# Kernel tuning notes

Hardware: AMD Instinct MI355X
Metric: run time of the kernel (lower is better)

The kernel has to match this reference:

```python
import jax, jax.numpy as jnp
import numpy as np

C = 256
EPS = 1e-5


def setup_inputs() -> dict:
    key = jax.random.key(0)
    ks = jax.random.split(key, 10)
    B, H, W = 4, 64, 64
    x1 = jax.random.normal(ks[0], (B, C, H, W), dtype=jnp.float32)
    x2 = jax.random.normal(ks[1], (B, C, H, W), dtype=jnp.float32)
    s = 1.0 / np.sqrt(C)
    qw = jax.random.normal(ks[2], (C, C), dtype=jnp.float32) * s
    qb = jax.random.normal(ks[3], (C,), dtype=jnp.float32) * 0.01
    kw = jax.random.normal(ks[4], (C, C), dtype=jnp.float32) * s
    kb = jax.random.normal(ks[5], (C,), dtype=jnp.float32) * 0.01
    vw = jax.random.normal(ks[6], (C, C), dtype=jnp.float32) * s
    vb = jax.random.normal(ks[7], (C,), dtype=jnp.float32) * 0.01
    ln_w = jnp.ones((C,), dtype=jnp.float32)
    ln_b = jnp.zeros((C,), dtype=jnp.float32)
    return {"x1": x1, "x2": x2, "qw": qw, "qb": qb, "kw": kw, "kb": kb,
            "vw": vw, "vb": vb, "ln_w": ln_w, "ln_b": ln_b}


def _conv1x1(x, w, b):
    # 1x1 conv == per-pixel matmul over channels. x: [B,C,H,W], w: [O,C]
    return jnp.einsum('oc,bchw->bohw', w, x) + b[None, :, None, None]


def reference(x1, x2, qw, qb, kw, kb, vw, vb, ln_w, ln_b):
    q = _conv1x1(x1, qw, qb)   # [B,C,H,W]
    k = _conv1x1(x2, kw, kb)   # [B,C,H,W]
    v = _conv1x1(x2, vw, vb)   # [B,C,H,W]
    # scores: [B,H,W,I,J]; softmax over LAST axis (j) only, as in the torch code
    scores = jnp.einsum('bchw,bcij->bhwij', q, k)
    attn = jax.nn.softmax(scores, axis=-1)
    fusion = jnp.einsum('bhwij,bcij->bchw', attn, v)  # [B,C,H,W]
    # LayerNorm2d: normalize over channel dim per spatial location
    mean = jnp.mean(fusion, axis=1, keepdims=True)
    var = jnp.var(fusion, axis=1, keepdims=True)
    normed = (fusion - mean) * jax.lax.rsqrt(var + EPS)
    return normed * ln_w[None, :, None, None] + ln_b[None, :, None, None]
```

## Files before the change

### kernel.cpp

```cpp
#include <hip/hip_runtime.h>


#define CDIM 256
#define NPOS 4096
#define BATCH 4
#define EPSV 1e-5f

typedef _Float16 f16;
typedef __attribute__((ext_vector_type(4))) _Float16 f16x4;
typedef __attribute__((ext_vector_type(8))) _Float16 f16x8;
typedef __attribute__((ext_vector_type(4))) float f32x4;
typedef __attribute__((ext_vector_type(16))) float f32x16;

#define WST       264
#define QK_STRIDE 264
#define V_STRIDE  72
#define DQ_STRIDE 72
#define F_STRIDE  68

#define LBAR() asm volatile("s_waitcnt lgkmcnt(0)\n\ts_barrier" ::: "memory")


static __device__ __forceinline__ f16x8 cvt8(const float* __restrict__ p) {
    float4 w0 = *(const float4*)p;
    float4 w1 = *(const float4*)(p + 4);
    f16x8 r;
    r[0] = (f16)w0.x; r[1] = (f16)w0.y; r[2] = (f16)w0.z; r[3] = (f16)w0.w;
    r[4] = (f16)w1.x; r[5] = (f16)w1.y; r[6] = (f16)w1.z; r[7] = (f16)w1.w;
    return r;
}

__global__ __launch_bounds__(256, 4) void prep_kernel(
    const float* __restrict__ x1, const float* __restrict__ x2,
    const float* __restrict__ qw, const float* __restrict__ kw,
    const float* __restrict__ vw,
    f16* __restrict__ X1T, f16* __restrict__ X2T, f16* __restrict__ W16)
{
    const int id = blockIdx.x;
    const int t  = threadIdx.x;
    if (id < 2048) {
        __shared__ f16 T[64 * 72];
        const float* xs = (id & 1) ? x2 : x1;
        f16* dst        = (id & 1) ? X2T : X1T;
        const int t2 = id >> 1;
        const int b  = t2 >> 8;
        const int rm = t2 & 255;
        const int c0 = (rm >> 6) * 64;
        const int n0 = (rm & 63) * 64;
        const float* src = xs + ((size_t)b * CDIM + c0) * NPOS + n0;
        const int rr = t >> 6, col = t & 63;
        #pragma unroll
        for (int j = 0; j < 16; ++j) {
            int row = rr + j * 4;
            T[col * 72 + row] = (f16)src[(size_t)row * NPOS + col];
        }
        __syncthreads();
        const int n = t >> 3, lc = (t & 7) * 8;
        f16* d0 = dst + ((size_t)b * NPOS + n0) * CDIM + c0;
        #pragma unroll
        for (int j = 0; j < 2; ++j) {
            int nn = n + j * 32;
            *(f16x8*)(d0 + (size_t)nn * CDIM + lc) = *(const f16x8*)&T[nn * 72 + lc];
        }
    } else {
        const int wblk = id - 2048;
        const int pr = wblk >> 2, h = wblk & 3;
        const float* W = (pr == 0 ? qw : pr == 1 ? kw : vw) + (size_t)h * 64 * CDIM;
        f16* D = W16 + (size_t)pr * CDIM * CDIM + (size_t)h * 64 * CDIM;
        #pragma unroll
        for (int i = 0; i < 8; ++i) {
            int g = t + i * 256;
            int row = g >> 5, col = (g & 31) * 8;
            *(f16x8*)(D + (size_t)row * CDIM + col) = cvt8(W + (size_t)row * CDIM + col);
        }
    }
}

__global__ __launch_bounds__(256, 2) void gemm_kernel(
    const f16* __restrict__ X1T, const f16* __restrict__ X2T,
    const f16* __restrict__ W16,
    const float* __restrict__ qb, const float* __restrict__ kb,
    const float* __restrict__ vb,
    f16* __restrict__ Qg, f16* __restrict__ Kg, f16* __restrict__ Vg)
{
    __shared__ f16 Xs[64 * WST];
    __shared__ f16 Wh[64 * WST];
    __shared__ f16 Ds[64 * DQ_STRIDE];
    __shared__ float biasS[256];

    const int id = blockIdx.x;
    const int pr  = id >> 8;
    const int rem = id & 255;
    const int b   = rem >> 6;
    const int p0  = (rem & 63) << 6;
    const f16* XT = (pr == 0) ? X1T : X2T;
    const f16* Wp = W16 + (size_t)pr * CDIM * CDIM;
    const float* bias = pr == 0 ? qb : pr == 1 ? kb : vb;

    const int t = threadIdx.x, w = t >> 6, l = t & 63, lm = l & 31, lh = l >> 5;
    const int pt = w & 1, ot = w >> 1;

    biasS[t] = bias[t];
    #pragma unroll
    for (int it = 0; it < 8; ++it) {
        int p = w * 16 + it * 2 + lh;
        *(f16x8*)&Xs[p * WST + lm * 8] =
            *(const f16x8*)(XT + ((size_t)(b * NPOS + p0 + p)) * CDIM + lm * 8);
    }

    for (int q = 0; q < 4; ++q) {
        #pragma unroll
        for (int i = 0; i < 8; ++i) {
            int g = t + i * 256;
            int row = g >> 5, col = (g & 31) * 8;
            *(f16x8*)&Wh[row * WST + col] =
                *(const f16x8*)(Wp + (size_t)(q * 64 + row) * CDIM + col);
        }
        __syncthreads();

        f32x16 accA = {}, accB = {};
        #pragma unroll
        for (int ks = 0; ks < 16; ks += 2) {
            f16x8 x0 = *(const f16x8*)&Xs[(pt * 32 + lm) * WST + ks * 16 + lh * 8];
            f16x8 w0 = *(const f16x8*)&Wh[(ot * 32 + lm) * WST + ks * 16 + lh * 8];
            f16x8 x1v = *(const f16x8*)&Xs[(pt * 32 + lm) * WST + (ks + 1) * 16 + lh * 8];
            f16x8 w1 = *(const f16x8*)&Wh[(ot * 32 + lm) * WST + (ks + 1) * 16 + lh * 8];
            if (pr < 2) {
                accA = __builtin_amdgcn_mfma_f32_32x32x16_f16(x0, w0, accA, 0, 0, 0);
                accB = __builtin_amdgcn_mfma_f32_32x32x16_f16(x1v, w1, accB, 0, 0, 0);
            } else {
                accA = __builtin_amdgcn_mfma_f32_32x32x16_f16(w0, x0, accA, 0, 0, 0);
                accB = __builtin_amdgcn_mfma_f32_32x32x16_f16(w1, x1v, accB, 0, 0, 0);
            }
        }

        if (pr < 2) {
            int o_l = ot * 32 + lm;
            float bv = biasS[q * 64 + o_l];
            #pragma unroll
            for (int r = 0; r < 16; ++r) {
                int p_l = pt * 32 + (r & 3) + 8 * (r >> 2) + 4 * lh;
                Ds[p_l * DQ_STRIDE + o_l] = (f16)(accA[r] + accB[r] + bv);
            }
        } else {
            #pragma unroll
            for (int r = 0; r < 16; ++r) {
                int o_l = ot * 32 + (r & 3) + 8 * (r >> 2) + 4 * lh;
                Ds[o_l * DQ_STRIDE + pt * 32 + lm] =
                    (f16)(accA[r] + accB[r] + biasS[q * 64 + o_l]);
            }
        }
        __syncthreads();

        #pragma unroll
        for (int j = 0; j < 2; ++j) {
            int row = (t >> 3) + j * 32;
            int cc  = (t & 7) * 8;
            f16x8 vdat = *(const f16x8*)&Ds[row * DQ_STRIDE + cc];
            if (pr < 2) {
                f16* Out = (pr == 0) ? Qg : Kg;
                *(f16x8*)(Out + ((size_t)(b * NPOS + p0 + row)) * CDIM + q * 64 + cc) = vdat;
            } else {
                *(f16x8*)(Vg + ((size_t)(b * CDIM + q * 64 + row)) * NPOS + p0 + cc) = vdat;
            }
        }
        __syncthreads();
    }
}

__global__ __launch_bounds__(256, 2) void attn_kernel(
    const f16* __restrict__ Qg, const f16* __restrict__ Kg, const f16* __restrict__ Vg,
    float* __restrict__ Fp)
{
    __shared__ f16   Ks[64 * QK_STRIDE];
    __shared__ f16   Vs[256 * V_STRIDE];
    __shared__ f16   Pl[64 * V_STRIDE];
    __shared__ float RedM[2][64], RedS[2][64];

    const int t    = threadIdx.x;
    const int L    = (int)((blockIdx.x & 7) * 64 + (blockIdx.x >> 3));
    const int grp  = L >> 6;
    const int b    = grp >> 1;
    const int half = grp & 1;
    const int qt   = L & 63;
    const int p0   = qt << 6;
    const int bq   = b * 64 + qt;
    const int w    = t >> 6;
    const int l    = t & 63;
    const int lm   = l & 31;
    const int lh   = l >> 5;
    const int spt  = w & 1;
    const int skt  = w >> 1;

    f16x8 qf[16];
    {
        const f16* qptr = Qg + (size_t)(b * NPOS + p0 + spt * 32 + lm) * CDIM + lh * 8;
        #pragma unroll
        for (int ks = 0; ks < 16; ++ks) qf[ks] = *(const f16x8*)(qptr + ks * 16);
    }

    const int kr = t >> 5, koff = (t & 31) * 8;
    f16x8 kreg[8];
    auto issue_k = [&](int ch) {
        const int i0 = ch * 64;
        #pragma unroll
        for (int r = 0; r < 8; ++r)
            kreg[r] = *(const f16x8*)(Kg + (size_t)(b * NPOS + i0 + r * 8 + kr) * CDIM + koff);
    };

    const int vr = t >> 3;
    const int vc = (t & 7) * 8;
    f16x8 vreg[8];
    auto issue_v = [&](int ch) {
        const int i0 = ch * 64;
        #pragma unroll
        for (int i = 0; i < 8; ++i)
            vreg[i] = *(const f16x8*)(Vg + (size_t)(b * CDIM + i * 32 + vr) * NPOS + i0 + vc);
    };

    issue_k(half * 32);
    issue_v(half * 32);

    f32x16 facc[4] = {};

    for (int it = 0; it < 32; ++it) {
        const int ch = half * 32 + it;

        #pragma unroll
        for (int r = 0; r < 8; ++r)
            *(f16x8*)&Ks[(r * 8 + kr) * QK_STRIDE + koff] = kreg[r];
        if (it < 31) issue_k(ch + 1);
        LBAR();

        #pragma unroll
        for (int i = 0; i < 8; ++i)
            *(f16x8*)&Vs[(i * 32 + vr) * V_STRIDE + vc] = vreg[i];
        if (it < 31) issue_v(ch + 1);

        f32x16 st = {};
        __builtin_amdgcn_s_setprio(1);
        #pragma unroll
        for (int ks = 0; ks < 16; ++ks) {
            f16x8 kf = *(const f16x8*)&Ks[(skt * 32 + lm) * QK_STRIDE + ks * 16 + lh * 8];
            st = __builtin_amdgcn_mfma_f32_32x32x16_f16(kf, qf[ks], st, 0, 0, 0);
        }
        __builtin_amdgcn_s_setprio(0);

        float mx = st[0];
        #pragma unroll
        for (int r = 1; r < 16; ++r) mx = fmaxf(mx, st[r]);
        mx = fmaxf(mx, __shfl_xor(mx, 32));
        float ss = 0.f;
        #pragma unroll
        for (int r = 0; r < 16; ++r) {
            float e = __expf(st[r] - mx);
            st[r] = e;
            ss += e;
        }
        ss += __shfl_xor(ss, 32);
        if (lh == 0) { RedM[skt][spt * 32 + lm] = mx; RedS[skt][spt * 32 + lm] = ss; }
        LBAR();

        float mo = RedM[skt ^ 1][spt * 32 + lm];
        float so = RedS[skt ^ 1][spt * 32 + lm];
        float M  = fmaxf(mx, mo);
        float S  = ss * __expf(mx - M) + so * __expf(mo - M);
        float scale = __expf(mx - M) * __builtin_amdgcn_rcpf(S);

        #pragma unroll
        for (int rq = 0; rq < 4; ++rq) {
            f16x4 pk;
            #pragma unroll
            for (int q2 = 0; q2 < 4; ++q2) pk[q2] = (f16)(st[rq * 4 + q2] * scale);
            *(f16x4*)&Pl[(spt * 32 + lm) * V_STRIDE + skt * 32 + rq * 8 + lh * 4] = pk;
        }
        LBAR();

        __builtin_amdgcn_s_setprio(1);
        #pragma unroll
        for (int kb = 0; kb < 4; ++kb) {
            f16x8 pf0 = *(const f16x8*)&Pl[lm * V_STRIDE + kb * 16 + lh * 8];
            f16x8 pf1 = *(const f16x8*)&Pl[(32 + lm) * V_STRIDE + kb * 16 + lh * 8];
            f16x8 va0 = *(const f16x8*)&Vs[(w * 64 + lm) * V_STRIDE + kb * 16 + lh * 8];
            f16x8 va1 = *(const f16x8*)&Vs[(w * 64 + 32 + lm) * V_STRIDE + kb * 16 + lh * 8];
            facc[0] = __builtin_amdgcn_mfma_f32_32x32x16_f16(va0, pf0, facc[0], 0, 0, 0);
            facc[1] = __builtin_amdgcn_mfma_f32_32x32x16_f16(va0, pf1, facc[1], 0, 0, 0);
            facc[2] = __builtin_amdgcn_mfma_f32_32x32x16_f16(va1, pf0, facc[2], 0, 0, 0);
            facc[3] = __builtin_amdgcn_mfma_f32_32x32x16_f16(va1, pf1, facc[3], 0, 0, 0);
        }
        __builtin_amdgcn_s_setprio(0);
    }

    float* dst = Fp + ((size_t)bq * 2 + half) * (CDIM * 64);
    #pragma unroll
    for (int ii = 0; ii < 2; ++ii)
        #pragma unroll
        for (int jj = 0; jj < 2; ++jj)
            #pragma unroll
            for (int r = 0; r < 16; ++r) {
                int c = w * 64 + ii * 32 + (r & 3) + 8 * (r >> 2) + 4 * lh;
                int p = jj * 32 + lm;
                dst[c * 64 + p] = facc[ii * 2 + jj][r];
            }
}

__global__ __launch_bounds__(256, 2) void merge_ln_kernel(
    const float* __restrict__ Fp, const float* __restrict__ ln_w,
    const float* __restrict__ ln_b, float* __restrict__ out)
{
    __shared__ float Fs[256 * F_STRIDE];
    __shared__ float redS[16 * 64], redQ[16 * 64];
    __shared__ float lnw_s[256], lnb_s[256];
    __shared__ float mu_s[64], rs_s[64];

    const int t  = threadIdx.x;
    const int bq = blockIdx.x;
    const int b  = bq >> 6;
    const int p0 = (bq & 63) << 6;

    lnw_s[t] = ln_w[t]; lnb_s[t] = ln_b[t];

    const int pb = (t & 15) * 4;
    const int cg = t >> 4;
    const float* base = Fp + (size_t)bq * 2 * (CDIM * 64);

    f32x4 s4 = {}, q4 = {};
    #pragma unroll 4
    for (int ci = 0; ci < 16; ++ci) {
        int c = cg * 16 + ci;
        size_t off = (size_t)c * 64 + pb;
        f32x4 v = *(const f32x4*)(base + off);
        v += *(const f32x4*)(base + (size_t)(CDIM * 64) + off);
        *(f32x4*)&Fs[c * F_STRIDE + pb] = v;
        s4 += v; q4 += v * v;
    }
    #pragma unroll
    for (int k2 = 0; k2 < 4; ++k2) {
        redS[cg * 64 + pb + k2] = s4[k2];
        redQ[cg * 64 + pb + k2] = q4[k2];
    }
    __syncthreads();
    if (t < 64) {
        float ss = 0.f, qq = 0.f;
        #pragma unroll
        for (int g2 = 0; g2 < 16; ++g2) { ss += redS[g2 * 64 + t]; qq += redQ[g2 * 64 + t]; }
        float mean = ss * (1.0f / 256.0f);
        float var  = qq * (1.0f / 256.0f) - mean * mean;
        mu_s[t] = mean;
        rs_s[t] = rsqrtf(var + EPSV);
    }
    __syncthreads();
    const int p   = t & 63;
    const int cg2 = t >> 6;
    const float mu = mu_s[p], rs = rs_s[p];
    float* dst = out + (size_t)b * CDIM * NPOS + p0 + p;
    #pragma unroll 4
    for (int ci = 0; ci < 64; ++ci) {
        int c = cg2 * 64 + ci;
        dst[(size_t)c * NPOS] = (Fs[c * F_STRIDE + p] - mu) * rs * lnw_s[c] + lnb_s[c];
    }
}

extern "C" void kernel_launch(void* const* d_in, const int* in_sizes, int n_in,
                              void* d_out, int out_size, void* d_ws, size_t ws_size,
                              hipStream_t stream)
{
    const float* x1  = (const float*)d_in[0];
    const float* x2  = (const float*)d_in[1];
    const float* qw  = (const float*)d_in[2];
    const float* qb  = (const float*)d_in[3];
    const float* kw  = (const float*)d_in[4];
    const float* kb  = (const float*)d_in[5];
    const float* vw  = (const float*)d_in[6];
    const float* vb  = (const float*)d_in[7];
    const float* lnw = (const float*)d_in[8];
    const float* lnb = (const float*)d_in[9];

    const size_t tsz = (size_t)BATCH * NPOS * CDIM;
    f16* Qg  = (f16*)d_ws;
    f16* Kg  = Qg + tsz;
    f16* Vg  = Kg + tsz;
    f16* X1T = Vg + tsz;
    f16* X2T = X1T + tsz;
    f16* W16 = X2T + tsz;
    float* Fp = (float*)X1T;

    prep_kernel<<<2060, 256, 0, stream>>>(x1, x2, qw, kw, vw, X1T, X2T, W16);
    gemm_kernel<<<768, 256, 0, stream>>>(X1T, X2T, W16, qb, kb, vb, Qg, Kg, Vg);
    attn_kernel<<<512, 256, 0, stream>>>(Qg, Kg, Vg, Fp);
    merge_ln_kernel<<<256, 256, 0, stream>>>(Fp, lnw, lnb, (float*)d_out);
}
```

Measured before the change: 217.1 us.

## Store K and V pre-swizzled in MFMA fragment order and load directly from global

```diff
diff --git a/kernel.cpp b/kernel.cpp
--- a/kernel.cpp
+++ b/kernel.cpp
@@ -13,7 +13,6 @@
 typedef __attribute__((ext_vector_type(16))) float f32x16;
 
 #define WST       264
-#define QK_STRIDE 264
 #define V_STRIDE  72
 #define DQ_STRIDE 72
 #define F_STRIDE  68
@@ -81,7 +80,7 @@
     const f16* __restrict__ W16,
     const float* __restrict__ qb, const float* __restrict__ kb,
     const float* __restrict__ vb,
-    f16* __restrict__ Qg, f16* __restrict__ Kg, f16* __restrict__ Vg)
+    f16* __restrict__ Qg, f16* __restrict__ Kf, f16* __restrict__ Vf)
 {
     __shared__ f16 Xs[64 * WST];
     __shared__ f16 Wh[64 * WST];
@@ -152,16 +151,39 @@
         }
         __syncthreads();
 
-        #pragma unroll
-        for (int j = 0; j < 2; ++j) {
-            int row = (t >> 3) + j * 32;
-            int cc  = (t & 7) * 8;
-            f16x8 vdat = *(const f16x8*)&Ds[row * DQ_STRIDE + cc];
-            if (pr < 2) {
-                f16* Out = (pr == 0) ? Qg : Kg;
-                *(f16x8*)(Out + ((size_t)(b * NPOS + p0 + row)) * CDIM + q * 64 + cc) = vdat;
-            } else {
-                *(f16x8*)(Vg + ((size_t)(b * CDIM + q * 64 + row)) * NPOS + p0 + cc) = vdat;
+        if (pr == 0) {
+            #pragma unroll
+            for (int j = 0; j < 2; ++j) {
+                int row = (t >> 3) + j * 32;
+                int cc  = (t & 7) * 8;
+                f16x8 vdat = *(const f16x8*)&Ds[row * DQ_STRIDE + cc];
+                *(f16x8*)(Qg + ((size_t)(b * NPOS + p0 + row)) * CDIM + q * 64 + cc) = vdat;
+            }
+        } else if (pr == 1) {
+            #pragma unroll
+            for (int i = 0; i < 2; ++i) {
+                int idx  = t + i * 256;
+                int kt_l = idx >> 8;
+                int ks_l = (idx >> 6) & 3;
+                int l2   = idx & 63;
+                f16x8 vdat = *(const f16x8*)&Ds[(kt_l * 32 + (l2 & 31)) * DQ_STRIDE +
+                                                ks_l * 16 + (l2 >> 5) * 8];
+                size_t fo = (((size_t)b * 128 + (p0 >> 5) + kt_l) * 16 + q * 4 + ks_l) * 512
+                            + l2 * 8;
+                *(f16x8*)(Kf + fo) = vdat;
+            }
+        } else {
+            #pragma unroll
+            for (int i = 0; i < 2; ++i) {
+                int idx  = t + i * 256;
+                int ct_l = idx >> 8;
+                int kb_  = (idx >> 6) & 3;
+                int l2   = idx & 63;
+                f16x8 vdat = *(const f16x8*)&Ds[(ct_l * 32 + (l2 & 31)) * DQ_STRIDE +
+                                                kb_ * 16 + (l2 >> 5) * 8];
+                size_t fo = ((((size_t)b * 64 + (p0 >> 6)) * 8 + q * 2 + ct_l) * 4 + kb_) * 512
+                            + l2 * 8;
+                *(f16x8*)(Vf + fo) = vdat;
             }
         }
         __syncthreads();
@@ -169,13 +191,11 @@
 }
 
 __global__ __launch_bounds__(256, 2) void attn_kernel(
-    const f16* __restrict__ Qg, const f16* __restrict__ Kg, const f16* __restrict__ Vg,
+    const f16* __restrict__ Qg, const f16* __restrict__ Kf, const f16* __restrict__ Vf,
     float* __restrict__ Fp)
 {
-    __shared__ f16   Ks[64 * QK_STRIDE];
-    __shared__ f16   Vs[256 * V_STRIDE];
-    __shared__ f16   Pl[64 * V_STRIDE];
-    __shared__ float RedM[2][64], RedS[2][64];
+    __shared__ f16   Pl[2][64 * V_STRIDE];
+    __shared__ float RedM[2][2][64], RedS[2][2][64];
 
     const int t    = threadIdx.x;
     const int L    = (int)((blockIdx.x & 7) * 64 + (blockIdx.x >> 3));
@@ -199,49 +219,29 @@
         for (int ks = 0; ks < 16; ++ks) qf[ks] = *(const f16x8*)(qptr + ks * 16);
     }
 
-    const int kr = t >> 5, koff = (t & 31) * 8;
-    f16x8 kreg[8];
-    auto issue_k = [&](int ch) {
-        const int i0 = ch * 64;
-        #pragma unroll
-        for (int r = 0; r < 8; ++r)
-            kreg[r] = *(const f16x8*)(Kg + (size_t)(b * NPOS + i0 + r * 8 + kr) * CDIM + koff);
-    };
-
-    const int vr = t >> 3;
-    const int vc = (t & 7) * 8;
-    f16x8 vreg[8];
-    auto issue_v = [&](int ch) {
-        const int i0 = ch * 64;
-        #pragma unroll
-        for (int i = 0; i < 8; ++i)
-            vreg[i] = *(const f16x8*)(Vg + (size_t)(b * CDIM + i * 32 + vr) * NPOS + i0 + vc);
-    };
-
-    issue_k(half * 32);
-    issue_v(half * 32);
+    const f16* Kfb = Kf + (size_t)b * 128 * 16 * 512;
+    const f16* Vfb = Vf + (size_t)b * 64 * 8 * 4 * 512;
 
     f32x16 facc[4] = {};
 
     for (int it = 0; it < 32; ++it) {
         const int ch = half * 32 + it;
-
-        #pragma unroll
-        for (int r = 0; r < 8; ++r)
-            *(f16x8*)&Ks[(r * 8 + kr) * QK_STRIDE + koff] = kreg[r];
-        if (it < 31) issue_k(ch + 1);
-        LBAR();
-
-        #pragma unroll
-        for (int i = 0; i < 8; ++i)
-            *(f16x8*)&Vs[(i * 32 + vr) * V_STRIDE + vc] = vreg[i];
-        if (it < 31) issue_v(ch + 1);
-
+        const int pb = it & 1;
+
+        const f16* Vt = Vfb + (size_t)ch * 8 * 4 * 512;
+        f16x8 vf0[4], vf1[4];
+        #pragma unroll
+        for (int kb = 0; kb < 4; ++kb) {
+            vf0[kb] = *(const f16x8*)(Vt + (size_t)((2 * w) * 4 + kb) * 512 + l * 8);
+            vf1[kb] = *(const f16x8*)(Vt + (size_t)((2 * w + 1) * 4 + kb) * 512 + l * 8);
+        }
+
+        const f16* Kt = Kfb + (size_t)(ch * 2 + skt) * 16 * 512;
         f32x16 st = {};
         __builtin_amdgcn_s_setprio(1);
         #pragma unroll
         for (int ks = 0; ks < 16; ++ks) {
-            f16x8 kf = *(const f16x8*)&Ks[(skt * 32 + lm) * QK_STRIDE + ks * 16 + lh * 8];
+            f16x8 kf = *(const f16x8*)(Kt + (size_t)ks * 512 + l * 8);
             st = __builtin_amdgcn_mfma_f32_32x32x16_f16(kf, qf[ks], st, 0, 0, 0);
         }
         __builtin_amdgcn_s_setprio(0);
@@ -258,11 +258,11 @@
             ss += e;
         }
         ss += __shfl_xor(ss, 32);
-        if (lh == 0) { RedM[skt][spt * 32 + lm] = mx; RedS[skt][spt * 32 + lm] = ss; }
+        if (lh == 0) { RedM[pb][skt][spt * 32 + lm] = mx; RedS[pb][skt][spt * 32 + lm] = ss; }
         LBAR();
 
-        float mo = RedM[skt ^ 1][spt * 32 + lm];
-        float so = RedS[skt ^ 1][spt * 32 + lm];
+        float mo = RedM[pb][skt ^ 1][spt * 32 + lm];
+        float so = RedS[pb][skt ^ 1][spt * 32 + lm];
         float M  = fmaxf(mx, mo);
         float S  = ss * __expf(mx - M) + so * __expf(mo - M);
         float scale = __expf(mx - M) * __builtin_amdgcn_rcpf(S);
@@ -272,21 +272,19 @@
             f16x4 pk;
             #pragma unroll
             for (int q2 = 0; q2 < 4; ++q2) pk[q2] = (f16)(st[rq * 4 + q2] * scale);
-            *(f16x4*)&Pl[(spt * 32 + lm) * V_STRIDE + skt * 32 + rq * 8 + lh * 4] = pk;
+            *(f16x4*)&Pl[pb][(spt * 32 + lm) * V_STRIDE + skt * 32 + rq * 8 + lh * 4] = pk;
         }
         LBAR();
 
         __builtin_amdgcn_s_setprio(1);
         #pragma unroll
         for (int kb = 0; kb < 4; ++kb) {
-            f16x8 pf0 = *(const f16x8*)&Pl[lm * V_STRIDE + kb * 16 + lh * 8];
-            f16x8 pf1 = *(const f16x8*)&Pl[(32 + lm) * V_STRIDE + kb * 16 + lh * 8];
-            f16x8 va0 = *(const f16x8*)&Vs[(w * 64 + lm) * V_STRIDE + kb * 16 + lh * 8];
-            f16x8 va1 = *(const f16x8*)&Vs[(w * 64 + 32 + lm) * V_STRIDE + kb * 16 + lh * 8];
-            facc[0] = __builtin_amdgcn_mfma_f32_32x32x16_f16(va0, pf0, facc[0], 0, 0, 0);
-            facc[1] = __builtin_amdgcn_mfma_f32_32x32x16_f16(va0, pf1, facc[1], 0, 0, 0);
-            facc[2] = __builtin_amdgcn_mfma_f32_32x32x16_f16(va1, pf0, facc[2], 0, 0, 0);
-            facc[3] = __builtin_amdgcn_mfma_f32_32x32x16_f16(va1, pf1, facc[3], 0, 0, 0);
+            f16x8 pf0 = *(const f16x8*)&Pl[pb][lm * V_STRIDE + kb * 16 + lh * 8];
+            f16x8 pf1 = *(const f16x8*)&Pl[pb][(32 + lm) * V_STRIDE + kb * 16 + lh * 8];
+            facc[0] = __builtin_amdgcn_mfma_f32_32x32x16_f16(vf0[kb], pf0, facc[0], 0, 0, 0);
+            facc[1] = __builtin_amdgcn_mfma_f32_32x32x16_f16(vf0[kb], pf1, facc[1], 0, 0, 0);
+            facc[2] = __builtin_amdgcn_mfma_f32_32x32x16_f16(vf1[kb], pf0, facc[2], 0, 0, 0);
+            facc[3] = __builtin_amdgcn_mfma_f32_32x32x16_f16(vf1[kb], pf1, facc[3], 0, 0, 0);
         }
         __builtin_amdgcn_s_setprio(0);
     }
@@ -378,15 +376,15 @@
 
     const size_t tsz = (size_t)BATCH * NPOS * CDIM;
     f16* Qg  = (f16*)d_ws;
-    f16* Kg  = Qg + tsz;
-    f16* Vg  = Kg + tsz;
-    f16* X1T = Vg + tsz;
+    f16* Kf  = Qg + tsz;
+    f16* Vf  = Kf + tsz;
+    f16* X1T = Vf + tsz;
     f16* X2T = X1T + tsz;
     f16* W16 = X2T + tsz;
     float* Fp = (float*)X1T;
 
     prep_kernel<<<2060, 256, 0, stream>>>(x1, x2, qw, kw, vw, X1T, X2T, W16);
-    gemm_kernel<<<768, 256, 0, stream>>>(X1T, X2T, W16, qb, kb, vb, Qg, Kg, Vg);
-    attn_kernel<<<512, 256, 0, stream>>>(Qg, Kg, Vg, Fp);
+    gemm_kernel<<<768, 256, 0, stream>>>(X1T, X2T, W16, qb, kb, vb, Qg, Kf, Vf);
+    attn_kernel<<<512, 256, 0, stream>>>(Qg, Kf, Vf, Fp);
     merge_ln_kernel<<<256, 256, 0, stream>>>(Fp, lnw, lnb, (float*)d_out);
 }
```

Result: slower. 231.5 us (+6.6%).

## Fuse fp16 transpose/convert prep into projection GEMM kernel

Applied to the files above, without the earlier changes.

```diff
diff --git a/kernel.cpp b/kernel.cpp
--- a/kernel.cpp
+++ b/kernel.cpp
@@ -30,55 +30,10 @@
     return r;
 }
 
-__global__ __launch_bounds__(256, 4) void prep_kernel(
+__global__ __launch_bounds__(256, 2) void gemm_kernel(
     const float* __restrict__ x1, const float* __restrict__ x2,
     const float* __restrict__ qw, const float* __restrict__ kw,
     const float* __restrict__ vw,
-    f16* __restrict__ X1T, f16* __restrict__ X2T, f16* __restrict__ W16)
-{
-    const int id = blockIdx.x;
-    const int t  = threadIdx.x;
-    if (id < 2048) {
-        __shared__ f16 T[64 * 72];
-        const float* xs = (id & 1) ? x2 : x1;
-        f16* dst        = (id & 1) ? X2T : X1T;
-        const int t2 = id >> 1;
-        const int b  = t2 >> 8;
-        const int rm = t2 & 255;
-        const int c0 = (rm >> 6) * 64;
-        const int n0 = (rm & 63) * 64;
-        const float* src = xs + ((size_t)b * CDIM + c0) * NPOS + n0;
-        const int rr = t >> 6, col = t & 63;
-        #pragma unroll
-        for (int j = 0; j < 16; ++j) {
-            int row = rr + j * 4;
-            T[col * 72 + row] = (f16)src[(size_t)row * NPOS + col];
-        }
-        __syncthreads();
-        const int n = t >> 3, lc = (t & 7) * 8;
-        f16* d0 = dst + ((size_t)b * NPOS + n0) * CDIM + c0;
-        #pragma unroll
-        for (int j = 0; j < 2; ++j) {
-            int nn = n + j * 32;
-            *(f16x8*)(d0 + (size_t)nn * CDIM + lc) = *(const f16x8*)&T[nn * 72 + lc];
-        }
-    } else {
-        const int wblk = id - 2048;
-        const int pr = wblk >> 2, h = wblk & 3;
-        const float* W = (pr == 0 ? qw : pr == 1 ? kw : vw) + (size_t)h * 64 * CDIM;
-        f16* D = W16 + (size_t)pr * CDIM * CDIM + (size_t)h * 64 * CDIM;
-        #pragma unroll
-        for (int i = 0; i < 8; ++i) {
-            int g = t + i * 256;
-            int row = g >> 5, col = (g & 31) * 8;
-            *(f16x8*)(D + (size_t)row * CDIM + col) = cvt8(W + (size_t)row * CDIM + col);
-        }
-    }
-}
-
-__global__ __launch_bounds__(256, 2) void gemm_kernel(
-    const f16* __restrict__ X1T, const f16* __restrict__ X2T,
-    const f16* __restrict__ W16,
     const float* __restrict__ qb, const float* __restrict__ kb,
     const float* __restrict__ vb,
     f16* __restrict__ Qg, f16* __restrict__ Kg, f16* __restrict__ Vg)
@@ -93,19 +48,21 @@
     const int rem = id & 255;
     const int b   = rem >> 6;
     const int p0  = (rem & 63) << 6;
-    const f16* XT = (pr == 0) ? X1T : X2T;
-    const f16* Wp = W16 + (size_t)pr * CDIM * CDIM;
-    const float* bias = pr == 0 ? qb : pr == 1 ? kb : vb;
+    const float* xsrc = ((pr == 0) ? x1 : x2) + (size_t)b * CDIM * NPOS + p0;
+    const float* Wfp  = (pr == 0) ? qw : (pr == 1) ? kw : vw;
+    const float* bias = (pr == 0) ? qb : (pr == 1) ? kb : vb;
 
     const int t = threadIdx.x, w = t >> 6, l = t & 63, lm = l & 31, lh = l >> 5;
     const int pt = w & 1, ot = w >> 1;
 
     biasS[t] = bias[t];
     #pragma unroll
-    for (int it = 0; it < 8; ++it) {
-        int p = w * 16 + it * 2 + lh;
-        *(f16x8*)&Xs[p * WST + lm * 8] =
-            *(const f16x8*)(XT + ((size_t)(b * NPOS + p0 + p)) * CDIM + lm * 8);
+    for (int g = 0; g < 8; ++g) {
+        f16x8 h;
+        #pragma unroll
+        for (int j = 0; j < 8; ++j)
+            h[j] = (f16)xsrc[(size_t)(w * 64 + g * 8 + j) * NPOS + l];
+        *(f16x8*)&Xs[l * WST + w * 64 + g * 8] = h;
     }
 
     for (int q = 0; q < 4; ++q) {
@@ -114,7 +71,7 @@
             int g = t + i * 256;
             int row = g >> 5, col = (g & 31) * 8;
             *(f16x8*)&Wh[row * WST + col] =
-                *(const f16x8*)(Wp + (size_t)(q * 64 + row) * CDIM + col);
+                cvt8(Wfp + (size_t)(q * 64 + row) * CDIM + col);
         }
         __syncthreads();
 
@@ -380,13 +337,9 @@
     f16* Qg  = (f16*)d_ws;
     f16* Kg  = Qg + tsz;
     f16* Vg  = Kg + tsz;
-    f16* X1T = Vg + tsz;
-    f16* X2T = X1T + tsz;
-    f16* W16 = X2T + tsz;
-    float* Fp = (float*)X1T;
-
-    prep_kernel<<<2060, 256, 0, stream>>>(x1, x2, qw, kw, vw, X1T, X2T, W16);
-    gemm_kernel<<<768, 256, 0, stream>>>(X1T, X2T, W16, qb, kb, vb, Qg, Kg, Vg);
+    float* Fp = (float*)(Vg + tsz);
+
+    gemm_kernel<<<768, 256, 0, stream>>>(x1, x2, qw, kw, vw, qb, kb, vb, Qg, Kg, Vg);
     attn_kernel<<<512, 256, 0, stream>>>(Qg, Kg, Vg, Fp);
     merge_ln_kernel<<<256, 256, 0, stream>>>(Fp, lnw, lnb, (float*)d_out);
 }
```

New measurement: 218.5 us. No clear change (+0.6%).
